# Optimization experiments

Hardware: AMD Instinct MI355X
Metric: run time of the kernel (lower is better)

## Reference

```python
import jax, jax.numpy as jnp
import numpy as np

N_NODES, N_PARENTS, K_WORDS, MAX_DEG = 16384, 8192, 32, 4
VOCAB, HID, NCLASS = 100000, 64, 4
NEG_INF = -1e30


def setup_inputs() -> dict:
    key = jax.random.key(0)
    ks = jax.random.split(key, 16)
    L = N_NODES - N_PARENTS
    # tree: leaves-first node ordering; parent i is node L+i, children are earlier nodes
    rng = np.random.default_rng(0)
    tree = np.full((N_PARENTS, MAX_DEG + 1), -1, dtype=np.int32)
    for i in range(N_PARENTS):
        hi = L + i
        nc = int(rng.integers(1, MAX_DEG + 1))
        ch = rng.choice(hi, size=min(nc, hi), replace=False)
        tree[i, :len(ch)] = ch
        tree[i, MAX_DEG] = hi  # parent slot, ignored (row[:-1] used)
    s = 0.1
    return {
        "x_word": jax.random.uniform(ks[0], (N_NODES, K_WORDS), jnp.float32),
        "x_index": jax.random.randint(ks[1], (N_NODES, K_WORDS), 0, VOCAB, jnp.int32),
        "tree": jnp.asarray(tree),
        "E_bu": s * jax.random.normal(ks[2], (HID, VOCAB), jnp.float32),
        "W_z_bu": s * jax.random.normal(ks[3], (HID, HID), jnp.float32),
        "U_z_bu": s * jax.random.normal(ks[4], (HID, HID), jnp.float32),
        "b_z_bu": jnp.zeros((1, HID), jnp.float32),
        "W_r_bu": s * jax.random.normal(ks[5], (HID, HID), jnp.float32),
        "U_r_bu": s * jax.random.normal(ks[6], (HID, HID), jnp.float32),
        "b_r_bu": jnp.zeros((1, HID), jnp.float32),
        "W_h_bu": s * jax.random.normal(ks[7], (HID, HID), jnp.float32),
        "U_h_bu": s * jax.random.normal(ks[8], (HID, HID), jnp.float32),
        "b_h_bu": jnp.zeros((1, HID), jnp.float32),
        "W_attn": s * jax.random.normal(ks[9], (HID, HID), jnp.float32),
        "W_out_bu": s * jax.random.normal(ks[10], (NCLASS, HID), jnp.float32),
        "b_out_bu": jnp.zeros((NCLASS,), jnp.float32),
    }


def reference(x_word, x_index, tree, E_bu, W_z_bu, U_z_bu, b_z_bu,
              W_r_bu, U_r_bu, b_r_bu, W_h_bu, U_h_bu, b_h_bu,
              W_attn, W_out_bu, b_out_bu):
    N = x_word.shape[0]
    P = tree.shape[0]
    L = N - P  # leaves first
    H = E_bu.shape[0]
    # node embedding xe[n] = x_word[n] @ E_bu[:, x_index[n]].T  -> [N,H]
    Eg = E_bu.T[x_index]                       # [N,K,H] gather (memory-bound)
    xe = jnp.einsum('nk,nkh->nh', x_word, Eg)  # [N,H]
    # Leaf update: child_h = zeros -> attn uniform, h_tilde = 0
    z_l = jax.nn.sigmoid(xe[:L] @ W_z_bu.T + b_z_bu)
    c_l = jnp.tanh(xe[:L] @ W_h_bu.T + b_h_bu)
    leaf_h = (1.0 - z_l) * c_l                 # z*0 + (1-z)*c
    node_h0 = jnp.zeros((N, H), xe.dtype).at[:L].set(leaf_h)
    children = tree[:, :-1]                    # [P, D] child indices, -1 padded

    def step(node_h, inp):
        idx, ch = inp
        mask = ch > -1
        ci = jnp.where(mask, ch, 0)
        child_h = node_h[ci]                   # [D,H]
        pxe = xe[L + idx]                      # [H]
        # attn = softmax(sigmoid(parent_xe @ W_attn @ child_h.T)) over valid children
        logits = jax.nn.sigmoid(pxe @ (W_attn @ child_h.T))
        attn = jax.nn.softmax(jnp.where(mask, logits, NEG_INF))
        h_tilde = attn @ child_h               # [H]  (LayerNorm output discarded in original)
        z = jax.nn.sigmoid(pxe @ W_z_bu.T + h_tilde @ U_z_bu.T + b_z_bu[0])
        r = jax.nn.sigmoid(pxe @ W_r_bu.T + h_tilde @ U_r_bu.T + b_r_bu[0])
        c = jnp.tanh(pxe @ W_h_bu.T + (r * h_tilde) @ U_h_bu.T + b_h_bu[0])
        h = z * h_tilde + (1.0 - z) * c        # dropout in eval = identity
        return node_h.at[L + idx].set(h), None

    node_h, _ = jax.lax.scan(step, node_h0, (jnp.arange(P), children))
    final = jnp.max(node_h[L:], axis=0)        # [H]
    return jax.nn.softmax((W_out_bu * final).sum(axis=1) + b_out_bu)
```

## Files before the change

kernel.cpp:

```cpp
#include <hip/hip_runtime.h>
#include <math.h>

#define NN 16384
#define NP 8192
#define NL 8192
#define KW 32
#define VC 100000
#define SENT  0xFFFFFFFFu
#define NEVER 0xFFFFFFFEu
#define CLEAN_EPOCH 1000

__device__ __forceinline__ float sigmoidf_(float x){ return 1.0f/(1.0f+expf(-x)); }

__global__ void __launch_bounds__(256) k_setup(const float* __restrict__ E, float* __restrict__ ET,
    const float* __restrict__ Wz, const float* __restrict__ Wr, const float* __restrict__ Wh,
    const float* __restrict__ Uz, const float* __restrict__ Ur, const float* __restrict__ Uh,
    float* __restrict__ WT, float* __restrict__ node_h, int* done, int* g_rem, int et_blocks){
  __shared__ float tile[64][65];
  int b = blockIdx.x;
  int lane = threadIdx.x & 63, ty = threadIdx.x >> 6;
  if (b < et_blocks){
    int v0 = b*64;
    for (int h = ty; h < 64; h += 4){
      int v = v0 + lane;
      tile[h][lane] = (v < VC) ? E[(size_t)h*VC + v] : 0.f;
    }
    __syncthreads();
    for (int vv = ty; vv < 64; vv += 4){
      int v = v0 + vv;
      if (v < VC) ET[v*64 + lane] = tile[lane][vv];
    }
  } else if (b < et_blocks + 6){
    int m = b - et_blocks;
    const float* src = (m==0)?Wz:(m==1)?Wr:(m==2)?Wh:(m==3)?Uz:(m==4)?Ur:Uh;
    float* dst = WT + m*4096;
    for (int h = ty; h < 64; h += 4) tile[h][lane] = src[h*64 + lane];
    __syncthreads();
    for (int k = ty; k < 64; k += 4) dst[k*64 + lane] = tile[lane][k];
  } else if (b < et_blocks + 6 + 2048){
    size_t idx = (size_t)(b - et_blocks - 6)*256 + threadIdx.x;
    ((unsigned int*)node_h)[(size_t)NL*64 + idx] = SENT;
  } else {
    int idx = (b - et_blocks - 6 - 2048)*256 + threadIdx.x;
    if (idx < NP) done[idx] = 0;
    if (idx == 0) *g_rem = NP;
  }
}

__device__ __forceinline__ void node_body(int wid, int lane, float xev,
    const float* __restrict__ WzT, const float* __restrict__ WrT,
    const float* __restrict__ WhT, const float* __restrict__ Wa,
    const float* __restrict__ bz, const float* __restrict__ br,
    const float* __restrict__ bh,
    float* __restrict__ node_h, float* __restrict__ pz, float* __restrict__ pr,
    float* __restrict__ pc, float* __restrict__ qa){
  if (wid < NL){
    float az0=0.f, az1=0.f, ah0=0.f, ah1=0.f;
    #pragma unroll 8
    for (int k=0;k<64;k+=2){
      float x0 = __shfl(xev, k), x1 = __shfl(xev, k+1);
      az0 += x0 * WzT[k*64+lane];     az1 += x1 * WzT[(k+1)*64+lane];
      ah0 += x0 * WhT[k*64+lane];     ah1 += x1 * WhT[(k+1)*64+lane];
    }
    float z = sigmoidf_(az0+az1 + bz[lane]);
    float c = tanhf(ah0+ah1 + bh[lane]);
    node_h[wid*64+lane] = (1.f-z)*c;
  } else {
    int i = wid - NL;
    float az=0.f, ar=0.f, ah=0.f, aq=0.f;
    #pragma unroll 4
    for (int k=0;k<64;++k){
      float xk = __shfl(xev, k);
      az += xk * WzT[k*64+lane];
      ar += xk * WrT[k*64+lane];
      ah += xk * WhT[k*64+lane];
      aq += xk * Wa [k*64+lane];
    }
    pz[i*64+lane] = az + bz[lane];
    pr[i*64+lane] = ar + br[lane];
    pc[i*64+lane] = ah + bh[lane];
    qa[i*64+lane] = aq;
  }
}

__global__ void __launch_bounds__(256) k_xenode(const float* __restrict__ xw,
    const int* __restrict__ xi, const float* __restrict__ ET,
    const float* __restrict__ WzT, const float* __restrict__ WrT,
    const float* __restrict__ WhT, const float* __restrict__ Wa,
    const float* __restrict__ bz, const float* __restrict__ br,
    const float* __restrict__ bh,
    float* __restrict__ node_h, float* __restrict__ pz, float* __restrict__ pr,
    float* __restrict__ pc, float* __restrict__ qa){
  int wid = blockIdx.x*(blockDim.x>>6) + (threadIdx.x>>6);
  int lane = threadIdx.x & 63;
  if (wid >= NN) return;
  int   idxl = (lane < KW) ? xi[wid*KW + lane] : 0;
  float wl   = (lane < KW) ? xw[wid*KW + lane] : 0.f;
  float xev = 0.f;
  #pragma unroll 8
  for (int k = 0; k < KW; ++k){
    int   vk = __shfl(idxl, k);
    float wk = __shfl(wl,   k);
    xev += wk * ET[vk*64 + lane];
  }
  node_body(wid, lane, xev, WzT,WrT,WhT,Wa, bz,br,bh, node_h, pz,pr,pc, qa);
}

__global__ void __launch_bounds__(256) k_xenode_direct(const float* __restrict__ xw,
    const int* __restrict__ xi, const float* __restrict__ E,
    const float* __restrict__ WzT, const float* __restrict__ WrT,
    const float* __restrict__ WhT, const float* __restrict__ Wa,
    const float* __restrict__ bz, const float* __restrict__ br,
    const float* __restrict__ bh,
    float* __restrict__ node_h, float* __restrict__ pz, float* __restrict__ pr,
    float* __restrict__ pc, float* __restrict__ qa){
  int wid = blockIdx.x*(blockDim.x>>6) + (threadIdx.x>>6);
  int lane = threadIdx.x & 63;
  if (wid >= NN) return;
  const float* w = xw + wid*KW;
  const int*   v = xi + wid*KW;
  const float* Erow = E + (size_t)lane*VC;
  float xev = 0.f;
  for (int k = 0; k < KW; ++k) xev += w[k] * Erow[v[k]];
  node_body(wid, lane, xev, WzT,WrT,WhT,Wa, bz,br,bh, node_h, pz,pr,pc, qa);
}

__device__ __forceinline__ float gru_compute(int lane,
    int c0,int c1,int c2,int c3,
    float chv0,float chv1,float chv2,float chv3,
    float q, float pzv, float prv, float pcv,
    const float* __restrict__ UzT, const float* __restrict__ UrT,
    const float* __restrict__ UhT)
{
  float d0=q*chv0, d1=q*chv1, d2=q*chv2, d3=q*chv3;
  #pragma unroll
  for (int off=32; off; off>>=1){
    d0 += __shfl_xor(d0, off); d1 += __shfl_xor(d1, off);
    d2 += __shfl_xor(d2, off); d3 += __shfl_xor(d3, off);
  }
  float l0 = (c0>=0)? sigmoidf_(d0) : -1e30f;
  float l1 = (c1>=0)? sigmoidf_(d1) : -1e30f;
  float l2 = (c2>=0)? sigmoidf_(d2) : -1e30f;
  float l3 = (c3>=0)? sigmoidf_(d3) : -1e30f;
  float mx = fmaxf(fmaxf(l0,l1), fmaxf(l2,l3));
  float e0=expf(l0-mx), e1=expf(l1-mx), e2=expf(l2-mx), e3=expf(l3-mx);
  float inv = 1.f/(e0+e1+e2+e3);
  float ht = (e0*chv0 + e1*chv1 + e2*chv2 + e3*chv3)*inv;
  float az0=0.f, az1=0.f, ar0=0.f, ar1=0.f;
  #pragma unroll 8
  for (int k=0;k<64;k+=2){
    float h0 = __shfl(ht, k), h1 = __shfl(ht, k+1);
    az0 += h0 * UzT[k*64+lane];     az1 += h1 * UzT[(k+1)*64+lane];
    ar0 += h0 * UrT[k*64+lane];     ar1 += h1 * UrT[(k+1)*64+lane];
  }
  float z = sigmoidf_(pzv + az0+az1);
  float r = sigmoidf_(prv + ar0+ar1);
  float rh = r*ht;
  float ac0=0.f, ac1=0.f, ac2=0.f, ac3=0.f;
  #pragma unroll 8
  for (int k=0;k<64;k+=4){
    float r0 = __shfl(rh, k),   r1 = __shfl(rh, k+1);
    float r2 = __shfl(rh, k+2), r3 = __shfl(rh, k+3);
    ac0 += r0 * UhT[k*64+lane];     ac1 += r1 * UhT[(k+1)*64+lane];
    ac2 += r2 * UhT[(k+2)*64+lane]; ac3 += r3 * UhT[(k+3)*64+lane];
  }
  float cc = tanhf(pcv + (ac0+ac1)+(ac2+ac3));
  return z*ht + (1.f-z)*cc;
}

__global__ void __launch_bounds__(256) k_dflow(const int* __restrict__ tree,
    const float* __restrict__ qa, const float* __restrict__ pz,
    const float* __restrict__ pr, const float* __restrict__ pc,
    const float* __restrict__ UzT, const float* __restrict__ UrT,
    const float* __restrict__ UhT,
    float* node_h, int* done, int* g_rem)
{
  int w = threadIdx.x >> 6, lane = threadIdx.x & 63;
  int i = blockIdx.x*4 + w;
  if (i >= NP) return;
  const int* tr = tree + i*5;
  int c0=tr[0], c1=tr[1], c2=tr[2], c3=tr[3];
  float q   = qa[i*64+lane];
  float pzv = pz[i*64+lane];
  float prv = pr[i*64+lane];
  float pcv = pc[i*64+lane];
  unsigned int* nhu = (unsigned int*)node_h;
  float chv[4];
  bool ok = true;
  #pragma unroll
  for (int j=0;j<4;++j){
    int c = (j==0)?c0:(j==1)?c1:(j==2)?c2:c3;
    float v = 0.f;
    if (c >= 0 && c < NL){
      v = node_h[c*64+lane];
    } else if (c >= NL){
      unsigned int u = nhu[(size_t)c*64 + lane];
      int rounds = 0;
      while (__any((int)(u == SENT)) && rounds < (1<<16)){
        if (lane == 0){
          unsigned int s0 = atomicCAS(&nhu[(size_t)c*64], NEVER, NEVER);
          while (s0 == SENT && rounds < (1<<16)){
            __builtin_amdgcn_s_sleep(16);
            ++rounds;
            s0 = atomicCAS(&nhu[(size_t)c*64], NEVER, NEVER);
          }
        }
        rounds = __shfl(rounds, 0) + 1;
        if (u == SENT) u = atomicCAS(&nhu[(size_t)c*64 + lane], NEVER, NEVER);
        if (__any((int)(u == SENT))) __builtin_amdgcn_s_sleep(4);
      }
      if (__any((int)(u == SENT))) ok = false;
      v = __uint_as_float(u);
    }
    chv[j] = v;
  }
  if (!ok) return;
  float h = gru_compute(lane, c0,c1,c2,c3, chv[0],chv[1],chv[2],chv[3],
                        q, pzv, prv, pcv, UzT, UrT, UhT);
  atomicExch(&nhu[(size_t)(NL+i)*64 + lane], __float_as_uint(h));
  if (lane==0){ done[i] = 1; atomicAdd(g_rem, -1); }
}

__device__ __forceinline__ bool lvl_ready(int c, int lvl, const int* done){
  if (c < NL) return true;
  int e = done[c - NL];
  return (e > 0 && e < lvl);
}

__global__ void __launch_bounds__(256) k_cleanup(const int* __restrict__ tree,
    const float* __restrict__ qa, const float* __restrict__ pz,
    const float* __restrict__ pr, const float* __restrict__ pc,
    const float* __restrict__ UzT, const float* __restrict__ UrT,
    const float* __restrict__ UhT,
    float* node_h, int* done, int* g_rem)
{
  int rem = *g_rem;
  if (rem <= 0) return;
  __shared__ int cnt_s;
  int w = threadIdx.x >> 6, lane = threadIdx.x & 63;
  int epoch = CLEAN_EPOCH;
  while (rem > 0){
    if (threadIdx.x == 0) cnt_s = 0;
    __syncthreads();
    int my = 0;
    for (int i = w; i < NP; i += 4){
      if (done[i]) continue;
      const int* tr = tree + i*5;
      int c0=tr[0], c1=tr[1], c2=tr[2], c3=tr[3];
      if (!(lvl_ready(c0,epoch,done) && lvl_ready(c1,epoch,done)
         && lvl_ready(c2,epoch,done) && lvl_ready(c3,epoch,done))) continue;
      float chv0 = (c0>=0)? node_h[c0*64+lane] : 0.f;
      float chv1 = (c1>=0)? node_h[c1*64+lane] : 0.f;
      float chv2 = (c2>=0)? node_h[c2*64+lane] : 0.f;
      float chv3 = (c3>=0)? node_h[c3*64+lane] : 0.f;
      float h = gru_compute(lane, c0,c1,c2,c3, chv0,chv1,chv2,chv3,
                            qa[i*64+lane], pz[i*64+lane], pr[i*64+lane], pc[i*64+lane],
                            UzT, UrT, UhT);
      node_h[(size_t)(NL+i)*64+lane] = h;
      if (lane==0) done[i] = epoch;
      ++my;
    }
    if (lane==0 && my) atomicAdd(&cnt_s, my);
    __syncthreads();
    rem -= cnt_s;
    ++epoch;
    __syncthreads();
  }
}

__global__ void k_max1(const float* __restrict__ node_h, float* __restrict__ partial){
  __shared__ float sm[4][64];
  int lane = threadIdx.x & 63, w = threadIdx.x>>6;
  int base = NL + blockIdx.x*128;
  float m = -1e30f;
  for (int r = w; r < 128; r += 4)
    m = fmaxf(m, node_h[(size_t)(base+r)*64 + lane]);
  sm[w][lane] = m;
  __syncthreads();
  if (w==0){
    m = fmaxf(fmaxf(sm[0][lane],sm[1][lane]), fmaxf(sm[2][lane],sm[3][lane]));
    partial[blockIdx.x*64+lane] = m;
  }
}

__global__ void k_max2(const float* __restrict__ partial, const float* __restrict__ Wout,
                       const float* __restrict__ bout, float* __restrict__ out){
  int lane = threadIdx.x;
  float m = -1e30f;
  for (int b=0;b<64;++b) m = fmaxf(m, partial[b*64+lane]);
  float s0 = Wout[0*64+lane]*m;
  float s1 = Wout[1*64+lane]*m;
  float s2 = Wout[2*64+lane]*m;
  float s3 = Wout[3*64+lane]*m;
  #pragma unroll
  for (int off=32; off; off>>=1){
    s0 += __shfl_xor(s0, off);
    s1 += __shfl_xor(s1, off);
    s2 += __shfl_xor(s2, off);
    s3 += __shfl_xor(s3, off);
  }
  s0 += bout[0]; s1 += bout[1]; s2 += bout[2]; s3 += bout[3];
  float mx = fmaxf(fmaxf(s0,s1), fmaxf(s2,s3));
  float e0=expf(s0-mx), e1=expf(s1-mx), e2=expf(s2-mx), e3=expf(s3-mx);
  float inv = 1.f/(e0+e1+e2+e3);
  if (lane==0){
    out[0]=e0*inv; out[1]=e1*inv; out[2]=e2*inv; out[3]=e3*inv;
  }
}

__global__ void k_ws_sentinel(float* out, float wsmb){
  if (threadIdx.x < 4) out[threadIdx.x] = wsmb;
}

extern "C" void kernel_launch(void* const* d_in, const int* in_sizes, int n_in,
                              void* d_out, int out_size, void* d_ws, size_t ws_size,
                              hipStream_t stream){
  const float* x_word = (const float*)d_in[0];
  const int*   x_index= (const int*)d_in[1];
  const int*   tree   = (const int*)d_in[2];
  const float* E      = (const float*)d_in[3];
  const float* Wz     = (const float*)d_in[4];
  const float* Uz     = (const float*)d_in[5];
  const float* bz     = (const float*)d_in[6];
  const float* Wr     = (const float*)d_in[7];
  const float* Ur     = (const float*)d_in[8];
  const float* br     = (const float*)d_in[9];
  const float* Wh     = (const float*)d_in[10];
  const float* Uh     = (const float*)d_in[11];
  const float* bh     = (const float*)d_in[12];
  const float* Wa     = (const float*)d_in[13];
  const float* Wout   = (const float*)d_in[14];
  const float* bout   = (const float*)d_in[15];
  float* out = (float*)d_out;

  float* ws = (float*)d_ws;

  const size_t R0_FULL = 6400000;
  const size_t R0_FB   = 4096;
  const size_t TAIL    = 2097152 + 1048576 + 24576 + NP + 1;
  const size_t FULL_NEED = (R0_FULL + TAIL) * 4;
  const size_t FB_NEED   = (R0_FB   + TAIL) * 4;

  bool full = (ws_size >= FULL_NEED);
  bool fb   = (!full && ws_size >= FB_NEED);
  if (!full && !fb){
    k_ws_sentinel<<<1, 64, 0, stream>>>(out, (float)(ws_size >> 20));
    return;
  }

  float* ET   = ws;
  float* part = ws;
  size_t r0   = full ? R0_FULL : R0_FB;
  float* qa    = ws + r0;
  float* pz    = qa + 524288;
  float* pr    = pz + 524288;
  float* pc    = pr + 524288;
  float* nodeh = pc + 524288;
  float* WT    = nodeh + 1048576;
  int*   done  = (int*)(WT + 24576);
  int*   g_rem = done + NP;
  float* WzT = WT,       *WrT = WT+4096,  *WhT = WT+8192;
  float* UzT = WT+12288, *UrT = WT+16384, *UhT = WT+20480;

  int et_blocks = full ? (VC+63)/64 : 0;
  k_setup<<<et_blocks + 6 + 2048 + NP/256, 256, 0, stream>>>(
      E, ET, Wz, Wr, Wh, Uz, Ur, Uh, WT, nodeh, done, g_rem, et_blocks);
  if (full)
    k_xenode<<<NN/4, 256, 0, stream>>>(x_word, x_index, ET, WzT, WrT, WhT, Wa,
                                       bz, br, bh, nodeh, pz, pr, pc, qa);
  else
    k_xenode_direct<<<NN/4, 256, 0, stream>>>(x_word, x_index, E, WzT, WrT, WhT, Wa,
                                              bz, br, bh, nodeh, pz, pr, pc, qa);
  k_dflow  <<<NP/4, 256, 0, stream>>>(tree, qa, pz, pr, pc, UzT, UrT, UhT,
                                      nodeh, done, g_rem);
  k_cleanup<<<1,    256, 0, stream>>>(tree, qa, pz, pr, pc, UzT, UrT, UhT,
                                      nodeh, done, g_rem);
  k_max1   <<<64,   256, 0, stream>>>(nodeh, part);
  k_max2   <<<1,     64, 0, stream>>>(part, Wout, bout, out);
}
```

Baseline: 184.0 us.

## Fuse node embedding kernel with dataflow GRU tree kernel

Merges the embedding/projection kernel and the dataflow tree-GRU kernel into one launch. Leaves now publish their states with atomic exchange over sentinel-initialized storage, so parents can consume them without waiting for a kernel boundary. The child-wait loop polls all four children at once rather than one at a time. Because waves that are spinning may occupy CUs while their producers are still unscheduled, more parents may fall through to the single-block cleanup kernel, and all node states now have to be sentinel-initialized.

```diff
diff --git a/kernel.cpp b/kernel.cpp
--- a/kernel.cpp
+++ b/kernel.cpp
@@ -37,92 +37,14 @@
     for (int h = ty; h < 64; h += 4) tile[h][lane] = src[h*64 + lane];
     __syncthreads();
     for (int k = ty; k < 64; k += 4) dst[k*64 + lane] = tile[lane][k];
-  } else if (b < et_blocks + 6 + 2048){
+  } else if (b < et_blocks + 6 + 4096){
     size_t idx = (size_t)(b - et_blocks - 6)*256 + threadIdx.x;
-    ((unsigned int*)node_h)[(size_t)NL*64 + idx] = SENT;
+    ((unsigned int*)node_h)[idx] = SENT;
   } else {
-    int idx = (b - et_blocks - 6 - 2048)*256 + threadIdx.x;
+    int idx = (b - et_blocks - 6 - 4096)*256 + threadIdx.x;
     if (idx < NP) done[idx] = 0;
     if (idx == 0) *g_rem = NP;
   }
-}
-
-__device__ __forceinline__ void node_body(int wid, int lane, float xev,
-    const float* __restrict__ WzT, const float* __restrict__ WrT,
-    const float* __restrict__ WhT, const float* __restrict__ Wa,
-    const float* __restrict__ bz, const float* __restrict__ br,
-    const float* __restrict__ bh,
-    float* __restrict__ node_h, float* __restrict__ pz, float* __restrict__ pr,
-    float* __restrict__ pc, float* __restrict__ qa){
-  if (wid < NL){
-    float az0=0.f, az1=0.f, ah0=0.f, ah1=0.f;
-    #pragma unroll 8
-    for (int k=0;k<64;k+=2){
-      float x0 = __shfl(xev, k), x1 = __shfl(xev, k+1);
-      az0 += x0 * WzT[k*64+lane];     az1 += x1 * WzT[(k+1)*64+lane];
-      ah0 += x0 * WhT[k*64+lane];     ah1 += x1 * WhT[(k+1)*64+lane];
-    }
-    float z = sigmoidf_(az0+az1 + bz[lane]);
-    float c = tanhf(ah0+ah1 + bh[lane]);
-    node_h[wid*64+lane] = (1.f-z)*c;
-  } else {
-    int i = wid - NL;
-    float az=0.f, ar=0.f, ah=0.f, aq=0.f;
-    #pragma unroll 4
-    for (int k=0;k<64;++k){
-      float xk = __shfl(xev, k);
-      az += xk * WzT[k*64+lane];
-      ar += xk * WrT[k*64+lane];
-      ah += xk * WhT[k*64+lane];
-      aq += xk * Wa [k*64+lane];
-    }
-    pz[i*64+lane] = az + bz[lane];
-    pr[i*64+lane] = ar + br[lane];
-    pc[i*64+lane] = ah + bh[lane];
-    qa[i*64+lane] = aq;
-  }
-}
-
-__global__ void __launch_bounds__(256) k_xenode(const float* __restrict__ xw,
-    const int* __restrict__ xi, const float* __restrict__ ET,
-    const float* __restrict__ WzT, const float* __restrict__ WrT,
-    const float* __restrict__ WhT, const float* __restrict__ Wa,
-    const float* __restrict__ bz, const float* __restrict__ br,
-    const float* __restrict__ bh,
-    float* __restrict__ node_h, float* __restrict__ pz, float* __restrict__ pr,
-    float* __restrict__ pc, float* __restrict__ qa){
-  int wid = blockIdx.x*(blockDim.x>>6) + (threadIdx.x>>6);
-  int lane = threadIdx.x & 63;
-  if (wid >= NN) return;
-  int   idxl = (lane < KW) ? xi[wid*KW + lane] : 0;
-  float wl   = (lane < KW) ? xw[wid*KW + lane] : 0.f;
-  float xev = 0.f;
-  #pragma unroll 8
-  for (int k = 0; k < KW; ++k){
-    int   vk = __shfl(idxl, k);
-    float wk = __shfl(wl,   k);
-    xev += wk * ET[vk*64 + lane];
-  }
-  node_body(wid, lane, xev, WzT,WrT,WhT,Wa, bz,br,bh, node_h, pz,pr,pc, qa);
-}
-
-__global__ void __launch_bounds__(256) k_xenode_direct(const float* __restrict__ xw,
-    const int* __restrict__ xi, const float* __restrict__ E,
-    const float* __restrict__ WzT, const float* __restrict__ WrT,
-    const float* __restrict__ WhT, const float* __restrict__ Wa,
-    const float* __restrict__ bz, const float* __restrict__ br,
-    const float* __restrict__ bh,
-    float* __restrict__ node_h, float* __restrict__ pz, float* __restrict__ pr,
-    float* __restrict__ pc, float* __restrict__ qa){
-  int wid = blockIdx.x*(blockDim.x>>6) + (threadIdx.x>>6);
-  int lane = threadIdx.x & 63;
-  if (wid >= NN) return;
-  const float* w = xw + wid*KW;
-  const int*   v = xi + wid*KW;
-  const float* Erow = E + (size_t)lane*VC;
-  float xev = 0.f;
-  for (int k = 0; k < KW; ++k) xev += w[k] * Erow[v[k]];
-  node_body(wid, lane, xev, WzT,WrT,WhT,Wa, bz,br,bh, node_h, pz,pr,pc, qa);
 }
 
 __device__ __forceinline__ float gru_compute(int lane,
@@ -168,57 +90,116 @@
   return z*ht + (1.f-z)*cc;
 }
 
-__global__ void __launch_bounds__(256) k_dflow(const int* __restrict__ tree,
-    const float* __restrict__ qa, const float* __restrict__ pz,
-    const float* __restrict__ pr, const float* __restrict__ pc,
-    const float* __restrict__ UzT, const float* __restrict__ UrT,
-    const float* __restrict__ UhT,
-    float* node_h, int* done, int* g_rem)
-{
-  int w = threadIdx.x >> 6, lane = threadIdx.x & 63;
-  int i = blockIdx.x*4 + w;
-  if (i >= NP) return;
+__device__ __forceinline__ void fused_body(int wid, int lane, float xev,
+    const float* __restrict__ WzT, const float* __restrict__ WrT,
+    const float* __restrict__ WhT, const float* __restrict__ Wa,
+    const float* __restrict__ bz, const float* __restrict__ br,
+    const float* __restrict__ bh,
+    const float* __restrict__ UzT, const float* __restrict__ UrT,
+    const float* __restrict__ UhT, const int* __restrict__ tree,
+    float* node_h, float* pz, float* pr, float* pc, float* qa,
+    int* done, int* g_rem)
+{
+  unsigned int* nhu = (unsigned int*)node_h;
+  if (wid < NL){
+    float az0=0.f, az1=0.f, ah0=0.f, ah1=0.f;
+    #pragma unroll 8
+    for (int k=0;k<64;k+=2){
+      float x0 = __shfl(xev, k), x1 = __shfl(xev, k+1);
+      az0 += x0 * WzT[k*64+lane];     az1 += x1 * WzT[(k+1)*64+lane];
+      ah0 += x0 * WhT[k*64+lane];     ah1 += x1 * WhT[(k+1)*64+lane];
+    }
+    float z = sigmoidf_(az0+az1 + bz[lane]);
+    float c = tanhf(ah0+ah1 + bh[lane]);
+    float h = (1.f-z)*c;
+    atomicExch(&nhu[(size_t)wid*64 + lane], __float_as_uint(h));
+    return;
+  }
+  int i = wid - NL;
+  float az=0.f, ar=0.f, ah=0.f, aq=0.f;
+  #pragma unroll 4
+  for (int k=0;k<64;++k){
+    float xk = __shfl(xev, k);
+    az += xk * WzT[k*64+lane];
+    ar += xk * WrT[k*64+lane];
+    ah += xk * WhT[k*64+lane];
+    aq += xk * Wa [k*64+lane];
+  }
+  float pzv = az + bz[lane], prv = ar + br[lane], pcv = ah + bh[lane], q = aq;
+  pz[i*64+lane] = pzv; pr[i*64+lane] = prv; pc[i*64+lane] = pcv; qa[i*64+lane] = q;
   const int* tr = tree + i*5;
   int c0=tr[0], c1=tr[1], c2=tr[2], c3=tr[3];
-  float q   = qa[i*64+lane];
-  float pzv = pz[i*64+lane];
-  float prv = pr[i*64+lane];
-  float pcv = pc[i*64+lane];
-  unsigned int* nhu = (unsigned int*)node_h;
-  float chv[4];
-  bool ok = true;
-  #pragma unroll
-  for (int j=0;j<4;++j){
-    int c = (j==0)?c0:(j==1)?c1:(j==2)?c2:c3;
-    float v = 0.f;
-    if (c >= 0 && c < NL){
-      v = node_h[c*64+lane];
-    } else if (c >= NL){
-      unsigned int u = nhu[(size_t)c*64 + lane];
-      int rounds = 0;
-      while (__any((int)(u == SENT)) && rounds < (1<<16)){
-        if (lane == 0){
-          unsigned int s0 = atomicCAS(&nhu[(size_t)c*64], NEVER, NEVER);
-          while (s0 == SENT && rounds < (1<<16)){
-            __builtin_amdgcn_s_sleep(16);
-            ++rounds;
-            s0 = atomicCAS(&nhu[(size_t)c*64], NEVER, NEVER);
-          }
-        }
-        rounds = __shfl(rounds, 0) + 1;
-        if (u == SENT) u = atomicCAS(&nhu[(size_t)c*64 + lane], NEVER, NEVER);
-        if (__any((int)(u == SENT))) __builtin_amdgcn_s_sleep(4);
-      }
-      if (__any((int)(u == SENT))) ok = false;
-      v = __uint_as_float(u);
-    }
-    chv[j] = v;
-  }
-  if (!ok) return;
-  float h = gru_compute(lane, c0,c1,c2,c3, chv[0],chv[1],chv[2],chv[3],
+  unsigned int u0 = (c0>=0)? nhu[(size_t)c0*64+lane] : 0u;
+  unsigned int u1 = (c1>=0)? nhu[(size_t)c1*64+lane] : 0u;
+  unsigned int u2 = (c2>=0)? nhu[(size_t)c2*64+lane] : 0u;
+  unsigned int u3 = (c3>=0)? nhu[(size_t)c3*64+lane] : 0u;
+  bool p0 = __any((int)(u0==SENT)), p1 = __any((int)(u1==SENT));
+  bool p2 = __any((int)(u2==SENT)), p3 = __any((int)(u3==SENT));
+  int rounds = 0;
+  while ((p0|p1|p2|p3) && rounds < (1<<16)){
+    if (p0){ if (u0==SENT) u0 = atomicCAS(&nhu[(size_t)c0*64+lane], NEVER, NEVER); p0 = __any((int)(u0==SENT)); }
+    if (p1){ if (u1==SENT) u1 = atomicCAS(&nhu[(size_t)c1*64+lane], NEVER, NEVER); p1 = __any((int)(u1==SENT)); }
+    if (p2){ if (u2==SENT) u2 = atomicCAS(&nhu[(size_t)c2*64+lane], NEVER, NEVER); p2 = __any((int)(u2==SENT)); }
+    if (p3){ if (u3==SENT) u3 = atomicCAS(&nhu[(size_t)c3*64+lane], NEVER, NEVER); p3 = __any((int)(u3==SENT)); }
+    if (p0|p1|p2|p3){ __builtin_amdgcn_s_sleep(4); ++rounds; }
+  }
+  if (p0|p1|p2|p3) return;
+  float h = gru_compute(lane, c0,c1,c2,c3,
+                        __uint_as_float(u0), __uint_as_float(u1),
+                        __uint_as_float(u2), __uint_as_float(u3),
                         q, pzv, prv, pcv, UzT, UrT, UhT);
   atomicExch(&nhu[(size_t)(NL+i)*64 + lane], __float_as_uint(h));
   if (lane==0){ done[i] = 1; atomicAdd(g_rem, -1); }
+}
+
+__global__ void __launch_bounds__(256) k_fused(const float* __restrict__ xw,
+    const int* __restrict__ xi, const float* __restrict__ ET,
+    const float* __restrict__ WzT, const float* __restrict__ WrT,
+    const float* __restrict__ WhT, const float* __restrict__ Wa,
+    const float* __restrict__ bz, const float* __restrict__ br,
+    const float* __restrict__ bh,
+    const float* __restrict__ UzT, const float* __restrict__ UrT,
+    const float* __restrict__ UhT, const int* __restrict__ tree,
+    float* node_h, float* pz, float* pr, float* pc, float* qa,
+    int* done, int* g_rem)
+{
+  int wid = blockIdx.x*4 + (threadIdx.x>>6);
+  int lane = threadIdx.x & 63;
+  if (wid >= NN) return;
+  int   idxl = (lane < KW) ? xi[wid*KW + lane] : 0;
+  float wl   = (lane < KW) ? xw[wid*KW + lane] : 0.f;
+  float xev = 0.f;
+  #pragma unroll 8
+  for (int k = 0; k < KW; ++k){
+    int   vk = __shfl(idxl, k);
+    float wk = __shfl(wl,   k);
+    xev += wk * ET[vk*64 + lane];
+  }
+  fused_body(wid, lane, xev, WzT,WrT,WhT,Wa, bz,br,bh, UzT,UrT,UhT, tree,
+             node_h, pz,pr,pc,qa, done, g_rem);
+}
+
+__global__ void __launch_bounds__(256) k_fused_direct(const float* __restrict__ xw,
+    const int* __restrict__ xi, const float* __restrict__ E,
+    const float* __restrict__ WzT, const float* __restrict__ WrT,
+    const float* __restrict__ WhT, const float* __restrict__ Wa,
+    const float* __restrict__ bz, const float* __restrict__ br,
+    const float* __restrict__ bh,
+    const float* __restrict__ UzT, const float* __restrict__ UrT,
+    const float* __restrict__ UhT, const int* __restrict__ tree,
+    float* node_h, float* pz, float* pr, float* pc, float* qa,
+    int* done, int* g_rem)
+{
+  int wid = blockIdx.x*4 + (threadIdx.x>>6);
+  int lane = threadIdx.x & 63;
+  if (wid >= NN) return;
+  const float* w = xw + wid*KW;
+  const int*   v = xi + wid*KW;
+  const float* Erow = E + (size_t)lane*VC;
+  float xev = 0.f;
+  for (int k = 0; k < KW; ++k) xev += w[k] * Erow[v[k]];
+  fused_body(wid, lane, xev, WzT,WrT,WhT,Wa, bz,br,bh, UzT,UrT,UhT, tree,
+             node_h, pz,pr,pc,qa, done, g_rem);
 }
 
 __device__ __forceinline__ bool lvl_ready(int c, int lvl, const int* done){
@@ -363,18 +344,18 @@
   float* UzT = WT+12288, *UrT = WT+16384, *UhT = WT+20480;
 
   int et_blocks = full ? (VC+63)/64 : 0;
-  k_setup<<<et_blocks + 6 + 2048 + NP/256, 256, 0, stream>>>(
+  k_setup<<<et_blocks + 6 + 4096 + NP/256, 256, 0, stream>>>(
       E, ET, Wz, Wr, Wh, Uz, Ur, Uh, WT, nodeh, done, g_rem, et_blocks);
   if (full)
-    k_xenode<<<NN/4, 256, 0, stream>>>(x_word, x_index, ET, WzT, WrT, WhT, Wa,
-                                       bz, br, bh, nodeh, pz, pr, pc, qa);
+    k_fused<<<NN/4, 256, 0, stream>>>(x_word, x_index, ET, WzT, WrT, WhT, Wa,
+                                      bz, br, bh, UzT, UrT, UhT, tree,
+                                      nodeh, pz, pr, pc, qa, done, g_rem);
   else
-    k_xenode_direct<<<NN/4, 256, 0, stream>>>(x_word, x_index, E, WzT, WrT, WhT, Wa,
-                                              bz, br, bh, nodeh, pz, pr, pc, qa);
-  k_dflow  <<<NP/4, 256, 0, stream>>>(tree, qa, pz, pr, pc, UzT, UrT, UhT,
-                                      nodeh, done, g_rem);
-  k_cleanup<<<1,    256, 0, stream>>>(tree, qa, pz, pr, pc, UzT, UrT, UhT,
-                                      nodeh, done, g_rem);
-  k_max1   <<<64,   256, 0, stream>>>(nodeh, part);
-  k_max2   <<<1,     64, 0, stream>>>(part, Wout, bout, out);
-}
+    k_fused_direct<<<NN/4, 256, 0, stream>>>(x_word, x_index, E, WzT, WrT, WhT, Wa,
+                                             bz, br, bh, UzT, UrT, UhT, tree,
+                                             nodeh, pz, pr, pc, qa, done, g_rem);
+  k_cleanup<<<1,  256, 0, stream>>>(tree, qa, pz, pr, pc, UzT, UrT, UhT,
+                                    nodeh, done, g_rem);
+  k_max1   <<<64, 256, 0, stream>>>(nodeh, part);
+  k_max2   <<<1,   64, 0, stream>>>(part, Wout, bout, out);
+}
```

New measurement: 164.1 us. -10.8%, faster.
